# Performance work log

Measured on AMD Instinct MI355X. Metric: run time of the kernel, lower is better.

## Reference

```python
import jax, jax.numpy as jnp
import numpy as np

DIM_MODEL = 2048
DQK = 64
DV = 64
NUM_HEADS = 32
NUM_GROUPS = 8
H_PER_G = NUM_HEADS // NUM_GROUPS
ROPE_THETA = 10000.0
RMS_EPS = 1e-6


def _rope(x):
    # x: [b, g, h, s, d]; rotate-half RoPE over last dim, positions along s.
    d = x.shape[-1]
    s = x.shape[-2]
    inv_freq = 1.0 / (ROPE_THETA ** (jnp.arange(0, d, 2, dtype=jnp.float32) / d))  # [d/2]
    ang = jnp.arange(s, dtype=jnp.float32)[:, None] * inv_freq[None, :]  # [s, d/2]
    cos, sin = jnp.cos(ang), jnp.sin(ang)
    x1, x2 = x[..., : d // 2], x[..., d // 2 :]
    return jnp.concatenate([x1 * cos - x2 * sin, x2 * cos + x1 * sin], axis=-1)


def setup_inputs() -> dict:
    key = jax.random.key(0)
    k1, k2, k3 = jax.random.split(key, 3)
    b, s = 2, 2048
    concat = NUM_HEADS * DQK + NUM_GROUPS * (DQK + DV)  # 3072
    x = jax.random.normal(k1, (b, s, DIM_MODEL), dtype=jnp.float32)
    w_in = jax.random.normal(k2, (concat, DIM_MODEL), dtype=jnp.float32) * (DIM_MODEL ** -0.5)
    w_out = jax.random.normal(k3, (DIM_MODEL, NUM_HEADS * DV), dtype=jnp.float32) * ((NUM_HEADS * DV) ** -0.5)
    rms_w = jnp.ones((DIM_MODEL,), dtype=jnp.float32)
    return {"x": x, "w_in": w_in, "w_out": w_out, "rms_w": rms_w}


def reference(x, w_in, w_out, rms_w):
    b, s, _ = x.shape
    # RMSNorm
    y = x * jax.lax.rsqrt(jnp.mean(x * x, axis=-1, keepdims=True) + RMS_EPS) * rms_w
    # In-projection (Linear, no bias): y @ w_in.T
    y = jnp.einsum('bsm,cm->bsc', y, w_in)
    cq = NUM_HEADS * DQK
    ck = NUM_GROUPS * DQK
    q, k, v = y[..., :cq], y[..., cq:cq + ck], y[..., cq + ck:]
    # q: b s (g h d) -> b g h s d ; k,v: b s (g d) -> b g 1 s d
    q = q.reshape(b, s, NUM_GROUPS, H_PER_G, DQK).transpose(0, 2, 3, 1, 4)
    k = k.reshape(b, s, NUM_GROUPS, DQK).transpose(0, 2, 1, 3)[:, :, None]
    v = v.reshape(b, s, NUM_GROUPS, DV).transpose(0, 2, 1, 3)[:, :, None]
    q = _rope(q)
    k = _rope(k)
    # scores with GQA broadcast over h
    qk = jnp.einsum('bghsd,bgxpd->bghsp', q, k) * (DQK ** -0.5)
    causal = jnp.tril(jnp.ones((s, s), dtype=bool))
    qk = jnp.where(causal, qk, -jnp.inf)
    attn = jax.nn.softmax(qk, axis=-1)
    o = jnp.einsum('bghsp,bgxpd->bghsd', attn, v)  # [b,g,h,s,d]
    o = o.transpose(0, 3, 1, 2, 4).reshape(b, s, NUM_HEADS * DV)
    y = jnp.einsum('bsc,mc->bsm', o, w_out)
    return x + y
```

## Files before the change

### kernel.cpp

```cpp
#include <hip/hip_runtime.h>
#include <hip/hip_bf16.h>

#define TOKENS   4096
#define SEQ      2048
#define DMODEL   2048
#define CONCAT   3072
#define NHEADS   32
#define NGROUPS  8
#define HPERG    4
#define CQ       2048
#define CK       512

typedef __attribute__((ext_vector_type(8))) short bf16x8;
typedef __attribute__((ext_vector_type(4))) float f32x4;

__device__ __forceinline__ ushort f2bf(float f) {
    __hip_bfloat16 h = __float2bfloat16(f);
    return __builtin_bit_cast(ushort, h);
}

#define GLOBAL_TO_LDS16(g, l)                                                  \
    __builtin_amdgcn_global_load_lds(                                          \
        (const __attribute__((address_space(1))) void*)(g),                    \
        (__attribute__((address_space(3))) void*)(l), 16, 0, 0)

__global__ void rmsnorm_kernel(const float* __restrict__ x,
                               const float* __restrict__ w,
                               ushort* __restrict__ y_bf) {
    int t = blockIdx.x;
    const float4* xr = (const float4*)(x + (size_t)t * DMODEL);
    float4 v[2];
    float ss = 0.f;
#pragma unroll
    for (int i = 0; i < 2; i++) {
        v[i] = xr[threadIdx.x + i * 256];
        ss += v[i].x * v[i].x + v[i].y * v[i].y + v[i].z * v[i].z + v[i].w * v[i].w;
    }
#pragma unroll
    for (int off = 32; off >= 1; off >>= 1) ss += __shfl_xor(ss, off);
    __shared__ float red[4];
    int wid = threadIdx.x >> 6;
    if ((threadIdx.x & 63) == 0) red[wid] = ss;
    __syncthreads();
    float total = red[0] + red[1] + red[2] + red[3];
    float scale = rsqrtf(total * (1.0f / DMODEL) + 1e-6f);
    const float4* wr = (const float4*)w;
    ushort4* yr = (ushort4*)(y_bf + (size_t)t * DMODEL);
#pragma unroll
    for (int i = 0; i < 2; i++) {
        int c = threadIdx.x + i * 256;
        float4 wv = wr[c];
        ushort4 o;
        o.x = f2bf(v[i].x * scale * wv.x);
        o.y = f2bf(v[i].y * scale * wv.y);
        o.z = f2bf(v[i].z * scale * wv.z);
        o.w = f2bf(v[i].w * scale * wv.w);
        yr[c] = o;
    }
}

__global__ void pack_bf16_kernel(const float* __restrict__ src,
                                 ushort* __restrict__ dst, int n4) {
    int i = blockIdx.x * 256 + threadIdx.x;
    if (i < n4) {
        float4 v = ((const float4*)src)[i];
        ushort4 o;
        o.x = f2bf(v.x); o.y = f2bf(v.y); o.z = f2bf(v.z); o.w = f2bf(v.w);
        ((ushort4*)dst)[i] = o;
    }
}

template <bool EPILOGUE>
__global__ __launch_bounds__(256) void gemm_nt_mfma(
        const ushort* __restrict__ A, const ushort* __restrict__ B,
        float* __restrict__ C, const float* __restrict__ X,
        float* __restrict__ OUT, int M, int N, int K) {
    __shared__ __align__(16) ushort As[128 * 64];
    __shared__ __align__(16) ushort Bs[128 * 64];

    const int bm = blockIdx.y * 128, bn = blockIdx.x * 128;
    const int w = threadIdx.x >> 6, lane = threadIdx.x & 63;
    const int n = lane & 15, quad = lane >> 4;
    const int wr = (w & 1) * 64, wc = (w >> 1) * 64;

    const int r8 = lane >> 3;
    const int kb = (lane & 7) ^ r8;

    f32x4 acc[4][4] = {};

    for (int k0 = 0; k0 < K; k0 += 64) {
        __syncthreads();
#pragma unroll
        for (int i = 0; i < 4; i++) {
            int rbase = (w * 4 + i) * 8;
            const ushort* ga = A + (size_t)(bm + rbase + r8) * K + k0 + kb * 8;
            GLOBAL_TO_LDS16(ga, As + rbase * 64);
            const ushort* gb = B + (size_t)(bn + rbase + r8) * K + k0 + kb * 8;
            GLOBAL_TO_LDS16(gb, Bs + rbase * 64);
        }
        __syncthreads();

#pragma unroll
        for (int ks = 0; ks < 2; ks++) {
            bf16x8 af[4], bfr[4];
            int kblk = ks * 4 + quad;
#pragma unroll
            for (int mi = 0; mi < 4; mi++) {
                int row = wr + mi * 16 + n;
                af[mi] = *(const bf16x8*)(As + (row * 8 + (kblk ^ (row & 7))) * 8);
            }
#pragma unroll
            for (int ni = 0; ni < 4; ni++) {
                int row = wc + ni * 16 + n;
                bfr[ni] = *(const bf16x8*)(Bs + (row * 8 + (kblk ^ (row & 7))) * 8);
            }
#pragma unroll
            for (int mi = 0; mi < 4; mi++)
#pragma unroll
                for (int ni = 0; ni < 4; ni++)
                    acc[mi][ni] = __builtin_amdgcn_mfma_f32_16x16x32_bf16(
                        af[mi], bfr[ni], acc[mi][ni], 0, 0, 0);
        }
    }

#pragma unroll
    for (int mi = 0; mi < 4; mi++)
#pragma unroll
        for (int ni = 0; ni < 4; ni++)
#pragma unroll
            for (int r = 0; r < 4; r++) {
                int row = bm + wr + mi * 16 + quad * 4 + r;
                int col = bn + wc + ni * 16 + n;
                size_t idx = (size_t)row * N + col;
                float v = acc[mi][ni][r];
                if (EPILOGUE) OUT[idx] = X[idx] + v;
                else          C[idx]   = v;
            }
}

__global__ void pack_qk_kernel(const float* __restrict__ qkv,
                               __hip_bfloat16* __restrict__ Qb,
                               __hip_bfloat16* __restrict__ Kb) {
    int t = blockIdx.x;
    int b = t >> 11, s = t & (SEQ - 1);
    const float* row = qkv + (size_t)t * CONCAT;
    const float LOG2_THETA = 13.287712379549449f;
    const float QSCALE = 0.18033688011112042f;
    for (int i = threadIdx.x; i < CQ + CK; i += 256) {
        int head, d;
        const float* hb;
        if (i < CQ) { head = i >> 6; d = i & 63; hb = row + head * 64; }
        else { head = (i - CQ) >> 6; d = (i - CQ) & 63; hb = row + CQ + head * 64; }
        int j = d & 31;
        float inv = exp2f(-((float)j / 32.0f) * LOG2_THETA);
        float ang = (float)s * inv;
        float c = cosf(ang), sn = sinf(ang);
        float val;
        if (d < 32) val = hb[d] * c - hb[d + 32] * sn;
        else        val = hb[d] * c + hb[d - 32] * sn;
        if (i < CQ) val *= QSCALE;
        __hip_bfloat16 bv = __float2bfloat16(val);
        if (i < CQ) {
            int g = head >> 2, h = head & 3;
            Qb[((size_t)((b * 8 + g) * 4 + h) * SEQ + s) * 64 + d] = bv;
        } else {
            Kb[((size_t)(b * 8 + head) * SEQ + s) * 64 + d] = bv;
        }
    }
}

__global__ void pack_v_kernel(const float* __restrict__ qkv,
                              __hip_bfloat16* __restrict__ Vb) {
    int st = blockIdx.x & 31, bg = blockIdx.x >> 5;
    int b = bg >> 3, g = bg & 7;
    __shared__ float tile[64][65];
    int tid = threadIdx.x;
    int ls = tid >> 6;
    int d = tid & 63;
#pragma unroll
    for (int i = 0; i < 16; i++) {
        int s = st * 64 + i * 4 + ls;
        tile[i * 4 + ls][d] = qkv[(size_t)(b * SEQ + s) * CONCAT + CQ + CK + g * 64 + d];
    }
    __syncthreads();
#pragma unroll
    for (int i = 0; i < 16; i++) {
        int drow = i * 4 + ls;
        int scol = tid & 63;
        Vb[((size_t)(bg * 64 + drow)) * SEQ + st * 64 + scol] =
            __float2bfloat16(tile[scol][drow]);
    }
}

__global__ __launch_bounds__(256) void attn_mfma_kernel(
        const ushort* __restrict__ Qb, const ushort* __restrict__ Kb,
        const ushort* __restrict__ Vb, ushort* __restrict__ o_bf) {
    __shared__ __align__(16) ushort Kl[519 * 8];
    __shared__ __align__(16) ushort Vl[519 * 8];
    __shared__ __align__(16) uint   Pl[4][1056];

    int blk = blockIdx.x;
    int qt  = 15 - (blk >> 6);
    int bgh = blk & 63;
    int h = bgh & 3, g = (bgh >> 2) & 7, b = bgh >> 5;
    int w = threadIdx.x >> 6, lane = threadIdx.x & 63;
    int n = lane & 15, quad = lane >> 4;
    int Q0 = qt * 128;
    int qw = Q0 + w * 32;

    const ushort* Qh  = Qb + (size_t)((b * 8 + g) * 4 + h) * (SEQ * 64);
    const ushort* Kg0 = Kb + (size_t)(b * 8 + g) * (SEQ * 64);
    const ushort* Vg0 = Vb + (size_t)(b * 8 + g) * (64 * SEQ);

    bf16x8 aq[2][2];
#pragma unroll
    for (int qg = 0; qg < 2; qg++)
#pragma unroll
        for (int ks = 0; ks < 2; ks++)
            aq[qg][ks] = *(const bf16x8*)(
                Qh + (size_t)(qw + qg * 16 + n) * 64 + ks * 32 + quad * 8);

    f32x4 od[2][4] = {};
    f32x4 od4[2] = {};

    short onev = (n == 0) ? (short)0x3F80 : (short)0;
    bf16x8 bones = {onev, onev, onev, onev, onev, onev, onev, onev};

    uint* Pw = Pl[w];
    int nkt = qt * 2 + 2;
    for (int kt = 0; kt < nkt; kt++) {
        __syncthreads();
        {
            const ushort* Kg = Kg0 + kt * 64 * 64;
            const ushort* Vg = Vg0 + kt * 64;
#pragma unroll
            for (int rep = 0; rep < 2; rep++) {
                int e = (rep * 256 + threadIdx.x) * 8;
                int key = e >> 6, dblk = (e >> 3) & 7;
                *(bf16x8*)(Kl + (dblk * 65 + key) * 8) = *(const bf16x8*)(Kg + e);
            }
#pragma unroll
            for (int rep = 0; rep < 2; rep++) {
                int e = (rep * 256 + threadIdx.x) * 8;
                int d = e >> 6, kin = e & 63;
                *(bf16x8*)(Vl + ((kin >> 3) * 65 + d) * 8) =
                    *(const bf16x8*)(Vg + (size_t)d * SEQ + kin);
            }
        }
        __syncthreads();

        bool act1 = (kt * 64 <= qw + 31);
        if (!act1) continue;
        bool act0 = (kt * 64 <= qw + 15);

#pragma unroll
        for (int t16k = 0; t16k < 4; t16k++) {
            bf16x8 kf0 = *(const bf16x8*)(Kl + ((0 + quad) * 65 + t16k * 16 + n) * 8);
            bf16x8 kf1 = *(const bf16x8*)(Kl + ((4 + quad) * 65 + t16k * 16 + n) * 8);
            int key0 = kt * 64 + t16k * 16 + quad * 4;
#pragma unroll
            for (int qg = 0; qg < 2; qg++) {
                if (qg == 0 && !act0) continue;
                f32x4 c = {};
                c = __builtin_amdgcn_mfma_f32_16x16x32_bf16(kf0, aq[qg][0], c, 0, 0, 0);
                c = __builtin_amdgcn_mfma_f32_16x16x32_bf16(kf1, aq[qg][1], c, 0, 0, 0);
                int qrow = qw + qg * 16 + n;
                float p[4];
                if (kt * 64 + 63 > qw + qg * 16) {
#pragma unroll
                    for (int r = 0; r < 4; r++)
                        p[r] = (key0 + r <= qrow) ? __builtin_amdgcn_exp2f(c[r]) : 0.f;
                } else {
#pragma unroll
                    for (int r = 0; r < 4; r++)
                        p[r] = __builtin_amdgcn_exp2f(c[r]);
                }
                uint d0 = ((uint)f2bf(p[1]) << 16) | f2bf(p[0]);
                uint d1 = ((uint)f2bf(p[3]) << 16) | f2bf(p[2]);
                int base = ((t16k * 2 + (quad >> 1)) * 33 + qg * 16 + n) * 4
                           + (quad & 1) * 2;
                Pw[base]     = d0;
                Pw[base + 1] = d1;
            }
        }

#pragma unroll
        for (int kb2 = 0; kb2 < 2; kb2++) {
            bf16x8 bv[4];
#pragma unroll
            for (int dt = 0; dt < 4; dt++)
                bv[dt] = *(const bf16x8*)(Vl + ((kb2 * 4 + quad) * 65 + dt * 16 + n) * 8);
#pragma unroll
            for (int qg = 0; qg < 2; qg++) {
                if (qg == 0 && !act0) continue;
                bf16x8 ap = *(const bf16x8*)(
                    (const ushort*)Pw + ((kb2 * 4 + quad) * 33 + qg * 16 + n) * 8);
#pragma unroll
                for (int dt = 0; dt < 4; dt++)
                    od[qg][dt] = __builtin_amdgcn_mfma_f32_16x16x32_bf16(
                        ap, bv[dt], od[qg][dt], 0, 0, 0);
                od4[qg] = __builtin_amdgcn_mfma_f32_16x16x32_bf16(
                    ap, bones, od4[qg], 0, 0, 0);
            }
        }
    }

#pragma unroll
    for (int qg = 0; qg < 2; qg++) {
        float linv[4];
#pragma unroll
        for (int r = 0; r < 4; r++) {
            float lv = __shfl(od4[qg][r], lane & 48);
            linv[r] = __builtin_amdgcn_rcpf(lv);
        }
#pragma unroll
        for (int dt = 0; dt < 4; dt++)
#pragma unroll
            for (int r = 0; r < 4; r++) {
                int q = qw + qg * 16 + quad * 4 + r;
                int col = (g * 4 + h) * 64 + dt * 16 + n;
                o_bf[(size_t)(b * SEQ + q) * DMODEL + col] =
                    f2bf(od[qg][dt][r] * linv[r]);
            }
    }
}

extern "C" void kernel_launch(void* const* d_in, const int* in_sizes, int n_in,
                              void* d_out, int out_size, void* d_ws, size_t ws_size,
                              hipStream_t stream) {
    const float* x     = (const float*)d_in[0];
    const float* w_in  = (const float*)d_in[1];
    const float* w_out = (const float*)d_in[2];
    const float* rms_w = (const float*)d_in[3];
    float* out = (float*)d_out;

    const size_t MB = 1024 * 1024;
    char* ws = (char*)d_ws;
    float*  qkv      = (float*)ws;
    ushort* y_bf     = (ushort*)(ws + 48 * MB);
    ushort* w_in_bf  = (ushort*)(ws + 64 * MB);
    ushort* Qb       = (ushort*)(ws + 48 * MB);
    ushort* Kb       = (ushort*)(ws + 64 * MB);
    ushort* Vb       = (ushort*)(ws + 68 * MB);
    ushort* o_bf     = (ushort*)ws;
    ushort* w_out_bf = (ushort*)(ws + 16 * MB);

    rmsnorm_kernel<<<TOKENS, 256, 0, stream>>>(x, rms_w, y_bf);
    pack_bf16_kernel<<<(CONCAT * DMODEL / 4 + 255) / 256, 256, 0, stream>>>(
        w_in, w_in_bf, CONCAT * DMODEL / 4);

    gemm_nt_mfma<false><<<dim3(CONCAT / 128, TOKENS / 128), 256, 0, stream>>>(
        y_bf, w_in_bf, qkv, nullptr, nullptr, TOKENS, CONCAT, DMODEL);

    pack_qk_kernel<<<TOKENS, 256, 0, stream>>>(qkv, (__hip_bfloat16*)Qb,
                                               (__hip_bfloat16*)Kb);
    pack_v_kernel<<<512, 256, 0, stream>>>(qkv, (__hip_bfloat16*)Vb);
    pack_bf16_kernel<<<(DMODEL * DMODEL / 4 + 255) / 256, 256, 0, stream>>>(
        w_out, w_out_bf, DMODEL * DMODEL / 4);

    attn_mfma_kernel<<<1024, 256, 0, stream>>>(Qb, Kb, Vb, o_bf);

    gemm_nt_mfma<true><<<dim3(DMODEL / 128, TOKENS / 128), 256, 0, stream>>>(
        o_bf, w_out_bf, nullptr, x, out, TOKENS, DMODEL, DMODEL);
}
```

Baseline: 326.9 us.

## Replace GEMM with 256x256 double-buffered 8-wave phased pipeline

Replaces the simple 128x128 bf16 MFMA GEMM with a 256x256-tile, 512-thread kernel that double-buffers LDS and splits each K-tile into four phases. Each phase interleaves LDS fragment reads, async global-to-LDS loads for upcoming half-tiles, and MFMA bursts under raised wave priority, with explicit waitcnt and barriers. The aim is to hide global load latency behind compute and raise data reuse per tile. The cost is a much larger LDS footprint (128KB), fewer blocks (e.g. 192 for the in-projection and 128 for the out-projection), and possible tail or occupancy effects.

```diff
diff --git a/kernel.cpp b/kernel.cpp
--- a/kernel.cpp
+++ b/kernel.cpp
@@ -70,72 +70,142 @@
     }
 }
 
+#define LGKM(nn) asm volatile("s_waitcnt lgkmcnt(" #nn ")" ::: "memory")
+#define VMC(nn)  asm volatile("s_waitcnt vmcnt(" #nn ")" ::: "memory")
+#define SBAR()   __builtin_amdgcn_s_barrier()
+#define SCHED0() __builtin_amdgcn_sched_barrier(0)
+#define PRIO(p)  __builtin_amdgcn_s_setprio(p)
+
+#define RD_A(mh)                                                              \
+    _Pragma("unroll") for (int mi = 0; mi < 4; mi++)                          \
+    _Pragma("unroll") for (int ks = 0; ks < 2; ks++)                          \
+        af[mi][ks] = *(const bf16x8*)(Ab +                                    \
+            ((arow0 + (mh) * 64 + mi * 16) * 8 +                              \
+             ((ks * 4 + quad) ^ an)) * 8);
+
+#define RD_B(nh)                                                              \
+    _Pragma("unroll") for (int ni = 0; ni < 2; ni++)                          \
+    _Pragma("unroll") for (int ks = 0; ks < 2; ks++)                          \
+        bfr[nh][ni][ks] = *(const bf16x8*)(Bb +                               \
+            ((brow0 + (nh) * 32 + ni * 16) * 8 +                              \
+             ((ks * 4 + quad) ^ an)) * 8);
+
+#define MMQ(mh, nh)                                                           \
+    _Pragma("unroll") for (int mi = 0; mi < 4; mi++)                          \
+    _Pragma("unroll") for (int ni = 0; ni < 2; ni++)                          \
+    _Pragma("unroll") for (int ks = 0; ks < 2; ks++)                          \
+        acc[(mh) * 4 + mi][(nh) * 2 + ni] =                                   \
+            __builtin_amdgcn_mfma_f32_16x16x32_bf16(af[mi][ks],               \
+                bfr[nh][ni][ks], acc[(mh) * 4 + mi][(nh) * 2 + ni], 0, 0, 0);
+
+#define ISSUE_HALF(H_)                                                        \
+    {                                                                         \
+        int H = (H_);                                                         \
+        if (H < 4 * NT) {                                                     \
+            int t2 = H >> 2, j2 = H & 3;                                      \
+            int k0 = t2 << 6;                                                 \
+            if (j2 == 0 || j2 == 3) {                                         \
+                int half = (j2 == 3);                                         \
+                ushort* lb = (ushort*)&As[t2 & 1][0];                         \
+                _Pragma("unroll") for (int c = 0; c < 2; c++) {               \
+                    int s = w * 2 + c;                                        \
+                    int row = (s >> 3) * 128 + half * 64 + (s & 7) * 8;       \
+                    const ushort* g = Aptr +                                  \
+                        (size_t)(bm + row + l8) * K + k0 + kb8;               \
+                    GLOBAL_TO_LDS16(g, lb + row * 64);                        \
+                }                                                             \
+            } else {                                                          \
+                int half = (j2 == 2);                                         \
+                ushort* lb = (ushort*)&Bs[t2 & 1][0];                         \
+                _Pragma("unroll") for (int c = 0; c < 2; c++) {               \
+                    int s = w * 2 + c;                                        \
+                    int row = (s >> 2) * 64 + half * 32 + (s & 3) * 8;        \
+                    const ushort* g = Bptr +                                  \
+                        (size_t)(bn + row + l8) * K + k0 + kb8;               \
+                    GLOBAL_TO_LDS16(g, lb + row * 64);                        \
+                }                                                             \
+            }                                                                 \
+        }                                                                     \
+    }
+
+#define TILE(t_, BUF)                                                         \
+    {                                                                         \
+        const ushort* Ab = &As[BUF][0];                                       \
+        const ushort* Bb = &Bs[BUF][0];                                       \
+                                                \
+        RD_A(0); RD_B(0);                                                     \
+        ISSUE_HALF(4 * (t_) + 7);                                             \
+        LGKM(8);                                                              \
+        SBAR(); LGKM(0); SCHED0();                                            \
+        PRIO(1); MMQ(0, 0); PRIO(0);                                          \
+        SBAR();                                                               \
+                                                   \
+        RD_B(1);                                                              \
+        ISSUE_HALF(4 * (t_) + 8);                                             \
+        SBAR(); LGKM(0); SCHED0();                                            \
+        PRIO(1); MMQ(0, 1); PRIO(0);                                          \
+        SBAR();                                                               \
+                                                   \
+        RD_A(1);                                                              \
+        ISSUE_HALF(4 * (t_) + 9);                                             \
+        SBAR(); LGKM(0); SCHED0();                                            \
+        PRIO(1); MMQ(1, 0); PRIO(0);                                          \
+        SBAR();                                                               \
+                           \
+        ISSUE_HALF(4 * (t_) + 10);                                            \
+        SBAR(); SCHED0();                                                     \
+        PRIO(1); MMQ(1, 1); PRIO(0);                                          \
+        if ((t_) + 2 < NT)        { VMC(6); }                                 \
+        else if ((t_) + 2 == NT)  { VMC(0); }                                 \
+        SBAR();                                                               \
+    }
+
 template <bool EPILOGUE>
-__global__ __launch_bounds__(256) void gemm_nt_mfma(
-        const ushort* __restrict__ A, const ushort* __restrict__ B,
+__global__ __launch_bounds__(512, 2) void gemm_nt_8ph(
+        const ushort* __restrict__ Aptr, const ushort* __restrict__ Bptr,
         float* __restrict__ C, const float* __restrict__ X,
         float* __restrict__ OUT, int M, int N, int K) {
-    __shared__ __align__(16) ushort As[128 * 64];
-    __shared__ __align__(16) ushort Bs[128 * 64];
-
-    const int bm = blockIdx.y * 128, bn = blockIdx.x * 128;
+    __shared__ __align__(16) ushort As[2][256 * 64];
+    __shared__ __align__(16) ushort Bs[2][256 * 64];
+
+    const int bm = blockIdx.y * 256, bn = blockIdx.x * 256;
     const int w = threadIdx.x >> 6, lane = threadIdx.x & 63;
     const int n = lane & 15, quad = lane >> 4;
-    const int wr = (w & 1) * 64, wc = (w >> 1) * 64;
-
-    const int r8 = lane >> 3;
-    const int kb = (lane & 7) ^ r8;
-
-    f32x4 acc[4][4] = {};
-
-    for (int k0 = 0; k0 < K; k0 += 64) {
-        __syncthreads();
-#pragma unroll
-        for (int i = 0; i < 4; i++) {
-            int rbase = (w * 4 + i) * 8;
-            const ushort* ga = A + (size_t)(bm + rbase + r8) * K + k0 + kb * 8;
-            GLOBAL_TO_LDS16(ga, As + rbase * 64);
-            const ushort* gb = B + (size_t)(bn + rbase + r8) * K + k0 + kb * 8;
-            GLOBAL_TO_LDS16(gb, Bs + rbase * 64);
-        }
-        __syncthreads();
-
-#pragma unroll
-        for (int ks = 0; ks < 2; ks++) {
-            bf16x8 af[4], bfr[4];
-            int kblk = ks * 4 + quad;
-#pragma unroll
-            for (int mi = 0; mi < 4; mi++) {
-                int row = wr + mi * 16 + n;
-                af[mi] = *(const bf16x8*)(As + (row * 8 + (kblk ^ (row & 7))) * 8);
-            }
-#pragma unroll
-            for (int ni = 0; ni < 4; ni++) {
-                int row = wc + ni * 16 + n;
-                bfr[ni] = *(const bf16x8*)(Bs + (row * 8 + (kblk ^ (row & 7))) * 8);
-            }
-#pragma unroll
-            for (int mi = 0; mi < 4; mi++)
-#pragma unroll
-                for (int ni = 0; ni < 4; ni++)
-                    acc[mi][ni] = __builtin_amdgcn_mfma_f32_16x16x32_bf16(
-                        af[mi], bfr[ni], acc[mi][ni], 0, 0, 0);
-        }
-    }
-
-#pragma unroll
-    for (int mi = 0; mi < 4; mi++)
-#pragma unroll
-        for (int ni = 0; ni < 4; ni++)
+    const int wm = w >> 2, wn = w & 3;
+    const int an = n & 7;
+    const int l8 = lane >> 3;
+    const int kb8 = ((lane & 7) ^ l8) * 8;
+    const int arow0 = wm * 128 + n;
+    const int brow0 = wn * 64 + n;
+    const int NT = K >> 6;
+
+    f32x4 acc[8][4] = {};
+    bf16x8 af[4][2], bfr[2][2][2];
+
+    ISSUE_HALF(0); ISSUE_HALF(1); ISSUE_HALF(2); ISSUE_HALF(3);
+    ISSUE_HALF(4); ISSUE_HALF(5); ISSUE_HALF(6);
+    VMC(6);
+    SBAR();
+
+    for (int tt = 0; tt < NT; tt += 2) {
+        TILE(tt, 0);
+        TILE(tt + 1, 1);
+    }
+
+#pragma unroll
+    for (int mi = 0; mi < 8; mi++)
+#pragma unroll
+        for (int ni = 0; ni < 4; ni++) {
+            int row = bm + wm * 128 + mi * 16 + quad * 4;
+            int col = bn + wn * 64 + ni * 16 + n;
 #pragma unroll
             for (int r = 0; r < 4; r++) {
-                int row = bm + wr + mi * 16 + quad * 4 + r;
-                int col = bn + wc + ni * 16 + n;
-                size_t idx = (size_t)row * N + col;
+                size_t idx = (size_t)(row + r) * N + col;
                 float v = acc[mi][ni][r];
                 if (EPILOGUE) OUT[idx] = X[idx] + v;
                 else          C[idx]   = v;
             }
+        }
 }
 
 __global__ void pack_qk_kernel(const float* __restrict__ qkv,
@@ -349,7 +419,7 @@
     pack_bf16_kernel<<<(CONCAT * DMODEL / 4 + 255) / 256, 256, 0, stream>>>(
         w_in, w_in_bf, CONCAT * DMODEL / 4);
 
-    gemm_nt_mfma<false><<<dim3(CONCAT / 128, TOKENS / 128), 256, 0, stream>>>(
+    gemm_nt_8ph<false><<<dim3(CONCAT / 256, TOKENS / 256), 512, 0, stream>>>(
         y_bf, w_in_bf, qkv, nullptr, nullptr, TOKENS, CONCAT, DMODEL);
 
     pack_qk_kernel<<<TOKENS, 256, 0, stream>>>(qkv, (__hip_bfloat16*)Qb,
@@ -360,6 +430,6 @@
 
     attn_mfma_kernel<<<1024, 256, 0, stream>>>(Qb, Kb, Vb, o_bf);
 
-    gemm_nt_mfma<true><<<dim3(DMODEL / 128, TOKENS / 128), 256, 0, stream>>>(
+    gemm_nt_8ph<true><<<dim3(DMODEL / 256, TOKENS / 256), 512, 0, stream>>>(
         o_bf, w_out_bf, nullptr, x, out, TOKENS, DMODEL, DMODEL);
 }
```

Result: no change. 328.1 us (+0.4%).
